# Performance work log

Hardware: AMD Instinct MI355X
Metric: run time of the kernel (lower is better)

Reference implementation:

```python
import jax, jax.numpy as jnp
import numpy as np

B, N, C = 2, 2048, 768
H = 12
HD = C // H  # 64


def setup_inputs() -> dict:
    key = jax.random.key(0)
    ks = jax.random.split(key, 6)
    s = 0.02
    x = jax.random.normal(ks[0], (B, N, C), dtype=jnp.float32)
    xpos = jnp.arange(B * N, dtype=jnp.int64).reshape(B, N) % N
    W_qkv = jax.random.normal(ks[1], (3 * C, C), dtype=jnp.float32) * s
    b_qkv = jnp.zeros((3 * C,), dtype=jnp.float32)
    W_proj = jax.random.normal(ks[2], (C, C), dtype=jnp.float32) * s
    b_proj = jnp.zeros((C,), dtype=jnp.float32)
    return {"x": x, "xpos": xpos, "W_qkv": W_qkv, "b_qkv": b_qkv,
            "W_proj": W_proj, "b_proj": b_proj}


def reference(x, xpos, W_qkv, b_qkv, W_proj, b_proj):
    # rope is None in this configuration -> xpos is unused, matching torch module.
    Bx, Nx, Cx = x.shape
    scale = (Cx // H) ** -0.5
    qkv = x @ W_qkv.T + b_qkv                     # [B, N, 3C]
    qkv = qkv.reshape(Bx, Nx, 3, H, HD)
    q = jnp.einsum('bnhd->bhnd', qkv[:, :, 0])    # [B, H, N, HD]
    k = jnp.einsum('bnhd->bhnd', qkv[:, :, 1])
    v = jnp.einsum('bnhd->bhnd', qkv[:, :, 2])
    attn = jnp.einsum('bhnd,bhmd->bhnm', q, k) * scale  # [B, H, N, N]
    attn = jax.nn.softmax(attn, axis=-1)
    out = jnp.einsum('bhnm,bhmd->bhnd', attn, v)  # [B, H, N, HD]
    out = jnp.einsum('bhnd->bnhd', out).reshape(Bx, Nx, Cx)
    return out @ W_proj.T + b_proj
```

## Files before the change

kernel.cpp:

```cpp
#include <hip/hip_runtime.h>
#include <hip/hip_bf16.h>


typedef _Float16 half8 __attribute__((ext_vector_type(8)));
typedef _Float16 half4_t __attribute__((ext_vector_type(4)));
typedef float floatx4 __attribute__((ext_vector_type(4)));

#define LDA 72
#define LDP 72
#define SCALE_LOG2E 0.1803368801111204f

constexpr int XH_OFF    = 0;
constexpr int WQKV_OFF  = XH_OFF + 4096 * 768;
constexpr int WPROJ_OFF = WQKV_OFF + 2304 * 768;
constexpr int QK_OFF    = WPROJ_OFF + 768 * 768;
constexpr int VTH_OFF   = QK_OFF + 4096 * 1536;

__device__ __forceinline__ void gl16(const _Float16* g, _Float16* l) {
  __builtin_amdgcn_global_load_lds(
      (const __attribute__((address_space(1))) unsigned int*)g,
      (__attribute__((address_space(3))) unsigned int*)l, 16, 0, 0);
}

__global__ __launch_bounds__(256) void cvt_all(const float* __restrict__ x,
                                               const float* __restrict__ wqkv,
                                               const float* __restrict__ wproj,
                                               _Float16* __restrict__ ws) {
  constexpr int n1 = 4096 * 768 / 4;
  constexpr int n2 = 2304 * 768 / 4;
  int i = blockIdx.x * 256 + threadIdx.x;
  const float* src; _Float16* dst; int j;
  if (i < n1)           { src = x;     dst = ws + XH_OFF;    j = i; }
  else if (i < n1 + n2) { src = wqkv;  dst = ws + WQKV_OFF;  j = i - n1; }
  else                  { src = wproj; dst = ws + WPROJ_OFF; j = i - n1 - n2; }
  floatx4 f = *(const floatx4*)(src + 4 * j);
  half4_t h;
  h[0] = (_Float16)f[0]; h[1] = (_Float16)f[1];
  h[2] = (_Float16)f[2]; h[3] = (_Float16)f[3];
  *(half4_t*)(dst + 4 * j) = h;
}

__global__ __launch_bounds__(256) void qkv_gemm(const _Float16* __restrict__ xh,
                                                const _Float16* __restrict__ wh,
                                                const float* __restrict__ bias,
                                                _Float16* __restrict__ qkh,
                                                _Float16* __restrict__ vth) {
  __shared__ __align__(16) _Float16 sA[128 * 64];
  __shared__ __align__(16) _Float16 sB[128 * 64];
  const int tid = threadIdx.x;
  const int nblk = blockIdx.x % 18, mblk = blockIdx.x / 18;
  const int lane = tid & 63, w = tid >> 6;
  const int lane15 = lane & 15, quad = lane >> 4;
  const int wm = w >> 1, wn = w & 1;
  const int lrow = lane >> 3, lchunk = lane & 7;

  const int Abase = mblk * 128 * 768;
  const int Bbase = nblk * 128 * 768;
  const int r0 = w * 32;

  floatx4 acc[4][4];
#pragma unroll
  for (int mt = 0; mt < 4; ++mt)
#pragma unroll
    for (int nt = 0; nt < 4; ++nt) acc[mt][nt] = (floatx4){0.f, 0.f, 0.f, 0.f};

  for (int kt = 0; kt < 12; ++kt) {
    if (kt) __syncthreads();
#pragma unroll
    for (int i = 0; i < 4; ++i) {
      int row = r0 + 8 * i + lrow;
      gl16(xh + Abase + row * 768 + kt * 64 + lchunk * 8, sA + (r0 + 8 * i) * 64);
      gl16(wh + Bbase + row * 768 + kt * 64 + lchunk * 8, sB + (r0 + 8 * i) * 64);
    }
    __syncthreads();
#pragma unroll
    for (int ks = 0; ks < 2; ++ks) {
      half8 af[4], bf[4];
#pragma unroll
      for (int mt = 0; mt < 4; ++mt)
        af[mt] = *(const half8*)(sA + (wm * 64 + mt * 16 + lane15) * 64 + ks * 32 + quad * 8);
#pragma unroll
      for (int nt = 0; nt < 4; ++nt)
        bf[nt] = *(const half8*)(sB + (wn * 64 + nt * 16 + lane15) * 64 + ks * 32 + quad * 8);
#pragma unroll
      for (int mt = 0; mt < 4; ++mt)
#pragma unroll
        for (int nt = 0; nt < 4; ++nt)
          acc[mt][nt] = __builtin_amdgcn_mfma_f32_16x16x32_f16(af[mt], bf[nt], acc[mt][nt], 0, 0, 0);
    }
  }

  const int mbase = mblk * 128 + wm * 64;
  const int nbase = nblk * 128 + wn * 64;
#pragma unroll
  for (int nt = 0; nt < 4; ++nt) {
    int cbase = nbase + nt * 16;
    float bv = bias[cbase + lane15];
    if (cbase < 1536) {
      int col = cbase + lane15;
      float sc = (cbase < 768) ? SCALE_LOG2E : 1.0f;
#pragma unroll
      for (int mt = 0; mt < 4; ++mt)
#pragma unroll
        for (int r = 0; r < 4; ++r) {
          int token = mbase + mt * 16 + quad * 4 + r;
          qkh[token * 1536 + col] = (_Float16)((acc[mt][nt][r] + bv) * sc);
        }
    } else {
      int dcol = cbase - 1536 + lane15;
      int h = dcol >> 6, d = dcol & 63;
#pragma unroll
      for (int mt = 0; mt < 4; ++mt) {
        int tok0 = mbase + mt * 16 + quad * 4;
        int b = tok0 >> 11, n0 = tok0 & 2047;
        int bh = b * 12 + h;
        half4_t hv;
#pragma unroll
        for (int r = 0; r < 4; ++r) hv[r] = (_Float16)(acc[mt][nt][r] + bv);
        *(half4_t*)(vth + (bh * 64 + d) * 2048 + n0) = hv;
      }
    }
  }
}

__global__ __launch_bounds__(256) void attn_fused(const _Float16* __restrict__ qkh,
                                                  const _Float16* __restrict__ vth,
                                                  _Float16* __restrict__ aoh) {
  __shared__ __align__(16) _Float16 sK[64 * LDA];
  __shared__ __align__(16) _Float16 sVT[64 * LDA];
  __shared__ __align__(16) _Float16 sP[4 * 16 * LDP];
  const int tid = threadIdx.x;
  const int bx = blockIdx.x;
  const int bh = bx % 24, qt = bx / 24;
  const int b = bh / 12, h = bh % 12;
  const int lane = tid & 63, w = tid >> 6;
  const int lane15 = lane & 15, quad = lane >> 4;
  const int chunk = tid & 7, rbase = tid >> 3;
  _Float16* sPw = sP + w * 16 * LDP;

  const int qkbase = b * 2048 * 1536 + h * 64;
  const int qrow = qt * 64 + w * 16 + lane15;
  half8 qa0 = *(const half8*)(qkh + qkbase + qrow * 1536 + quad * 8);
  half8 qa1 = *(const half8*)(qkh + qkbase + qrow * 1536 + 32 + quad * 8);

  const _Float16* kptr = qkh + qkbase + 768;
  const _Float16* vptr = vth + bh * 64 * 2048;

  floatx4 O[4];
#pragma unroll
  for (int dt = 0; dt < 4; ++dt) O[dt] = (floatx4){0.f, 0.f, 0.f, 0.f};
  float mrow = -3.0e38f, lrow = 0.f;

  for (int kt = 0; kt < 32; ++kt) {
    half8 tk[2], tv[2];
#pragma unroll
    for (int i = 0; i < 2; ++i) {
      int row = rbase + 32 * i;
      tk[i] = *(const half8*)(kptr + (kt * 64 + row) * 1536 + chunk * 8);
      tv[i] = *(const half8*)(vptr + row * 2048 + kt * 64 + chunk * 8);
    }
    if (kt) __syncthreads();
#pragma unroll
    for (int i = 0; i < 2; ++i) {
      int row = rbase + 32 * i;
      *(half8*)(sK + row * LDA + chunk * 8) = tk[i];
      *(half8*)(sVT + row * LDA + chunk * 8) = tv[i];
    }
    __syncthreads();

    floatx4 s[4];
#pragma unroll
    for (int nt = 0; nt < 4; ++nt) {
      half8 kf0 = *(const half8*)(sK + (nt * 16 + lane15) * LDA + quad * 8);
      half8 kf1 = *(const half8*)(sK + (nt * 16 + lane15) * LDA + 32 + quad * 8);
      floatx4 a = (floatx4){0.f, 0.f, 0.f, 0.f};
      a = __builtin_amdgcn_mfma_f32_16x16x32_f16(kf0, qa0, a, 0, 0, 0);
      a = __builtin_amdgcn_mfma_f32_16x16x32_f16(kf1, qa1, a, 0, 0, 0);
      s[nt] = a;
    }

    float tmax = s[0][0];
#pragma unroll
    for (int nt = 0; nt < 4; ++nt)
#pragma unroll
      for (int r = 0; r < 4; ++r) tmax = fmaxf(tmax, s[nt][r]);
    tmax = fmaxf(tmax, __shfl_xor(tmax, 16, 64));
    tmax = fmaxf(tmax, __shfl_xor(tmax, 32, 64));

    if (__any(tmax > mrow)) {
      float mnew = fmaxf(mrow, tmax);
      float alpha = exp2f(mrow - mnew);
      lrow *= alpha;
      mrow = mnew;
      float ar[4];
#pragma unroll
      for (int r = 0; r < 4; ++r) ar[r] = __shfl(alpha, 4 * quad + r, 64);
#pragma unroll
      for (int dt = 0; dt < 4; ++dt)
#pragma unroll
        for (int r = 0; r < 4; ++r) O[dt][r] *= ar[r];
    }

    float rsum = 0.f;
#pragma unroll
    for (int nt = 0; nt < 4; ++nt)
#pragma unroll
      for (int r = 0; r < 4; ++r) {
        float p = exp2f(s[nt][r] - mrow);
        s[nt][r] = p;
        rsum += p;
      }
    rsum += __shfl_xor(rsum, 16, 64);
    rsum += __shfl_xor(rsum, 32, 64);
    lrow += rsum;

#pragma unroll
    for (int nt = 0; nt < 4; ++nt) {
      half4_t hp;
#pragma unroll
      for (int r = 0; r < 4; ++r) hp[r] = (_Float16)s[nt][r];
      *(half4_t*)(sPw + lane15 * LDP + nt * 16 + quad * 4) = hp;
    }
    asm volatile("s_waitcnt lgkmcnt(0)" ::: "memory");

#pragma unroll
    for (int kk = 0; kk < 2; ++kk) {
      half8 pa = *(const half8*)(sPw + lane15 * LDP + kk * 32 + quad * 8);
#pragma unroll
      for (int dt = 0; dt < 4; ++dt) {
        half8 vb = *(const half8*)(sVT + (dt * 16 + lane15) * LDA + kk * 32 + quad * 8);
        O[dt] = __builtin_amdgcn_mfma_f32_16x16x32_f16(pa, vb, O[dt], 0, 0, 0);
      }
    }
  }

  float inv = 1.0f / lrow;
  float ir[4];
#pragma unroll
  for (int r = 0; r < 4; ++r) ir[r] = __shfl(inv, 4 * quad + r, 64);
#pragma unroll
  for (int dt = 0; dt < 4; ++dt)
#pragma unroll
    for (int r = 0; r < 4; ++r) {
      int tok = qt * 64 + w * 16 + quad * 4 + r;
      aoh[(b * 2048 + tok) * 768 + h * 64 + dt * 16 + lane15] = (_Float16)(O[dt][r] * ir[r]);
    }
}

__global__ __launch_bounds__(256) void proj_gemm(const _Float16* __restrict__ ah,
                                                 const _Float16* __restrict__ wh,
                                                 const float* __restrict__ bias,
                                                 float* __restrict__ out) {
  __shared__ __align__(16) _Float16 sA[128 * 64];
  __shared__ __align__(16) _Float16 sB[128 * 64];
  const int tid = threadIdx.x;
  const int nblk = blockIdx.x % 6, mblk = blockIdx.x / 6;
  const int lane = tid & 63, w = tid >> 6;
  const int lane15 = lane & 15, quad = lane >> 4;
  const int wm = w >> 1, wn = w & 1;
  const int lrow = lane >> 3, lchunk = lane & 7;

  const int Abase = mblk * 128 * 768;
  const int Bbase = nblk * 128 * 768;
  const int r0 = w * 32;

  floatx4 acc[4][4];
#pragma unroll
  for (int mt = 0; mt < 4; ++mt)
#pragma unroll
    for (int nt = 0; nt < 4; ++nt) acc[mt][nt] = (floatx4){0.f, 0.f, 0.f, 0.f};

  for (int kt = 0; kt < 12; ++kt) {
    if (kt) __syncthreads();
#pragma unroll
    for (int i = 0; i < 4; ++i) {
      int row = r0 + 8 * i + lrow;
      gl16(ah + Abase + row * 768 + kt * 64 + lchunk * 8, sA + (r0 + 8 * i) * 64);
      gl16(wh + Bbase + row * 768 + kt * 64 + lchunk * 8, sB + (r0 + 8 * i) * 64);
    }
    __syncthreads();
#pragma unroll
    for (int ks = 0; ks < 2; ++ks) {
      half8 af[4], bf[4];
#pragma unroll
      for (int mt = 0; mt < 4; ++mt)
        af[mt] = *(const half8*)(sA + (wm * 64 + mt * 16 + lane15) * 64 + ks * 32 + quad * 8);
#pragma unroll
      for (int nt = 0; nt < 4; ++nt)
        bf[nt] = *(const half8*)(sB + (wn * 64 + nt * 16 + lane15) * 64 + ks * 32 + quad * 8);
#pragma unroll
      for (int mt = 0; mt < 4; ++mt)
#pragma unroll
        for (int nt = 0; nt < 4; ++nt)
          acc[mt][nt] = __builtin_amdgcn_mfma_f32_16x16x32_f16(af[mt], bf[nt], acc[mt][nt], 0, 0, 0);
    }
  }

  const int mbase = mblk * 128 + wm * 64;
  const int nbase = nblk * 128 + wn * 64;
#pragma unroll
  for (int nt = 0; nt < 4; ++nt) {
    int col = nbase + nt * 16 + lane15;
    float bv = bias[col];
#pragma unroll
    for (int mt = 0; mt < 4; ++mt)
#pragma unroll
      for (int r = 0; r < 4; ++r) {
        int token = mbase + mt * 16 + quad * 4 + r;
        out[token * 768 + col] = acc[mt][nt][r] + bv;
      }
  }
}

extern "C" void kernel_launch(void* const* d_in, const int* in_sizes, int n_in,
                              void* d_out, int out_size, void* d_ws, size_t ws_size,
                              hipStream_t stream) {
  const float* x     = (const float*)d_in[0];
  const float* wqkv  = (const float*)d_in[2];
  const float* bqkv  = (const float*)d_in[3];
  const float* wproj = (const float*)d_in[4];
  const float* bproj = (const float*)d_in[5];
  float* out = (float*)d_out;

  _Float16* ws = (_Float16*)d_ws;
  _Float16* xh     = ws + XH_OFF;
  _Float16* wqkvh  = ws + WQKV_OFF;
  _Float16* wprojh = ws + WPROJ_OFF;
  _Float16* qkh    = ws + QK_OFF;
  _Float16* vth    = ws + VTH_OFF;
  _Float16* aoh    = xh;

  constexpr int total_v4 = (4096 * 768 + 2304 * 768 + 768 * 768) / 4;
  cvt_all<<<total_v4 / 256, 256, 0, stream>>>(x, wqkv, wproj, ws);
  qkv_gemm<<<32 * 18, 256, 0, stream>>>(xh, wqkvh, bqkv, qkh, vth);
  attn_fused<<<24 * 32, 256, 0, stream>>>(qkh, vth, aoh);
  proj_gemm<<<32 * 6, 256, 0, stream>>>(aoh, wprojh, bproj, out);
}
```

Before: 192.3 us.

## Split attention along keys with merge kernel, shrink GEMM M-tiles to 64

The attention kernel now uses 512-thread blocks covering 128 queries and splits the key range into two halves. Each block writes unnormalized partial outputs plus row max and sum to workspace, and a new merge kernel combines the halves with a log-sum-exp rescale. This halves the per-block serial key loop and shares each K/V tile across more queries. Both GEMMs switch to 64x128 tiles with twice as many blocks to improve occupancy and load balance. The cost is an extra kernel launch, extra partial-result traffic to global memory, fp16 rounding of the unnormalized partials, and lower per-block reuse in the GEMMs.

```diff
diff --git a/kernel.cpp b/kernel.cpp
--- a/kernel.cpp
+++ b/kernel.cpp
@@ -15,6 +15,8 @@
 constexpr int WPROJ_OFF = WQKV_OFF + 2304 * 768;
 constexpr int QK_OFF    = WPROJ_OFF + 768 * 768;
 constexpr int VTH_OFF   = QK_OFF + 4096 * 1536;
+constexpr int PO_OFF    = VTH_OFF + 24 * 64 * 2048;
+constexpr int PSTAT_OFF = PO_OFF + 2 * 24 * 2048 * 64;
 
 __device__ __forceinline__ void gl16(const _Float16* g, _Float16* l) {
   __builtin_amdgcn_global_load_lds(
@@ -45,56 +47,53 @@
                                                 const float* __restrict__ bias,
                                                 _Float16* __restrict__ qkh,
                                                 _Float16* __restrict__ vth) {
-  __shared__ __align__(16) _Float16 sA[128 * 64];
+  __shared__ __align__(16) _Float16 sA[64 * 64];
   __shared__ __align__(16) _Float16 sB[128 * 64];
   const int tid = threadIdx.x;
   const int nblk = blockIdx.x % 18, mblk = blockIdx.x / 18;
   const int lane = tid & 63, w = tid >> 6;
   const int lane15 = lane & 15, quad = lane >> 4;
-  const int wm = w >> 1, wn = w & 1;
   const int lrow = lane >> 3, lchunk = lane & 7;
 
-  const int Abase = mblk * 128 * 768;
-  const int Bbase = nblk * 128 * 768;
-  const int r0 = w * 32;
-
-  floatx4 acc[4][4];
+  floatx4 acc[4][2];
 #pragma unroll
   for (int mt = 0; mt < 4; ++mt)
 #pragma unroll
-    for (int nt = 0; nt < 4; ++nt) acc[mt][nt] = (floatx4){0.f, 0.f, 0.f, 0.f};
+    for (int nt = 0; nt < 2; ++nt) acc[mt][nt] = (floatx4){0.f, 0.f, 0.f, 0.f};
 
   for (int kt = 0; kt < 12; ++kt) {
     if (kt) __syncthreads();
 #pragma unroll
-    for (int i = 0; i < 4; ++i) {
-      int row = r0 + 8 * i + lrow;
-      gl16(xh + Abase + row * 768 + kt * 64 + lchunk * 8, sA + (r0 + 8 * i) * 64);
-      gl16(wh + Bbase + row * 768 + kt * 64 + lchunk * 8, sB + (r0 + 8 * i) * 64);
+    for (int i = 0; i < 6; ++i) {
+      int g = w * 48 + 8 * i;
+      if (g < 64)
+        gl16(xh + (mblk * 64 + g + lrow) * 768 + kt * 64 + lchunk * 8, sA + g * 64);
+      else
+        gl16(wh + (nblk * 128 + (g - 64) + lrow) * 768 + kt * 64 + lchunk * 8,
+             sB + (g - 64) * 64);
     }
     __syncthreads();
 #pragma unroll
     for (int ks = 0; ks < 2; ++ks) {
-      half8 af[4], bf[4];
-#pragma unroll
-      for (int mt = 0; mt < 4; ++mt)
-        af[mt] = *(const half8*)(sA + (wm * 64 + mt * 16 + lane15) * 64 + ks * 32 + quad * 8);
-#pragma unroll
-      for (int nt = 0; nt < 4; ++nt)
-        bf[nt] = *(const half8*)(sB + (wn * 64 + nt * 16 + lane15) * 64 + ks * 32 + quad * 8);
-#pragma unroll
-      for (int mt = 0; mt < 4; ++mt)
-#pragma unroll
-        for (int nt = 0; nt < 4; ++nt)
+      half8 af[4], bf[2];
+#pragma unroll
+      for (int mt = 0; mt < 4; ++mt)
+        af[mt] = *(const half8*)(sA + (mt * 16 + lane15) * 64 + ks * 32 + quad * 8);
+#pragma unroll
+      for (int nt = 0; nt < 2; ++nt)
+        bf[nt] = *(const half8*)(sB + (w * 32 + nt * 16 + lane15) * 64 + ks * 32 + quad * 8);
+#pragma unroll
+      for (int mt = 0; mt < 4; ++mt)
+#pragma unroll
+        for (int nt = 0; nt < 2; ++nt)
           acc[mt][nt] = __builtin_amdgcn_mfma_f32_16x16x32_f16(af[mt], bf[nt], acc[mt][nt], 0, 0, 0);
     }
   }
 
-  const int mbase = mblk * 128 + wm * 64;
-  const int nbase = nblk * 128 + wn * 64;
-#pragma unroll
-  for (int nt = 0; nt < 4; ++nt) {
-    int cbase = nbase + nt * 16;
+  const int mbase = mblk * 64;
+#pragma unroll
+  for (int nt = 0; nt < 2; ++nt) {
+    int cbase = nblk * 128 + w * 32 + nt * 16;
     float bv = bias[cbase + lane15];
     if (cbase < 1536) {
       int col = cbase + lane15;
@@ -123,23 +122,28 @@
   }
 }
 
-__global__ __launch_bounds__(256) void attn_fused(const _Float16* __restrict__ qkh,
+__global__ __launch_bounds__(512) void attn_fused(const _Float16* __restrict__ qkh,
                                                   const _Float16* __restrict__ vth,
-                                                  _Float16* __restrict__ aoh) {
+                                                  _Float16* __restrict__ pO,
+                                                  float* __restrict__ pM,
+                                                  float* __restrict__ pL) {
   __shared__ __align__(16) _Float16 sK[64 * LDA];
   __shared__ __align__(16) _Float16 sVT[64 * LDA];
-  __shared__ __align__(16) _Float16 sP[4 * 16 * LDP];
+  __shared__ __align__(16) _Float16 sP[8 * 16 * LDP];
   const int tid = threadIdx.x;
   const int bx = blockIdx.x;
-  const int bh = bx % 24, qt = bx / 24;
+  const int bh = bx % 24;
+  const int rest = bx / 24;
+  const int ks = rest & 1, qt = rest >> 1;
   const int b = bh / 12, h = bh % 12;
   const int lane = tid & 63, w = tid >> 6;
   const int lane15 = lane & 15, quad = lane >> 4;
   const int chunk = tid & 7, rbase = tid >> 3;
+  const int wq = w >> 2, ww = w & 3;
   _Float16* sPw = sP + w * 16 * LDP;
 
   const int qkbase = b * 2048 * 1536 + h * 64;
-  const int qrow = qt * 64 + w * 16 + lane15;
+  const int qrow = qt * 128 + wq * 64 + ww * 16 + lane15;
   half8 qa0 = *(const half8*)(qkh + qkbase + qrow * 1536 + quad * 8);
   half8 qa1 = *(const half8*)(qkh + qkbase + qrow * 1536 + 32 + quad * 8);
 
@@ -151,21 +155,13 @@
   for (int dt = 0; dt < 4; ++dt) O[dt] = (floatx4){0.f, 0.f, 0.f, 0.f};
   float mrow = -3.0e38f, lrow = 0.f;
 
-  for (int kt = 0; kt < 32; ++kt) {
-    half8 tk[2], tv[2];
-#pragma unroll
-    for (int i = 0; i < 2; ++i) {
-      int row = rbase + 32 * i;
-      tk[i] = *(const half8*)(kptr + (kt * 64 + row) * 1536 + chunk * 8);
-      tv[i] = *(const half8*)(vptr + row * 2048 + kt * 64 + chunk * 8);
-    }
-    if (kt) __syncthreads();
-#pragma unroll
-    for (int i = 0; i < 2; ++i) {
-      int row = rbase + 32 * i;
-      *(half8*)(sK + row * LDA + chunk * 8) = tk[i];
-      *(half8*)(sVT + row * LDA + chunk * 8) = tv[i];
-    }
+  const int kt0 = ks * 16;
+  for (int kt = kt0; kt < kt0 + 16; ++kt) {
+    half8 tk = *(const half8*)(kptr + (kt * 64 + rbase) * 1536 + chunk * 8);
+    half8 tv = *(const half8*)(vptr + rbase * 2048 + kt * 64 + chunk * 8);
+    if (kt != kt0) __syncthreads();
+    *(half8*)(sK + rbase * LDA + chunk * 8) = tk;
+    *(half8*)(sVT + rbase * LDA + chunk * 8) = tv;
     __syncthreads();
 
     floatx4 s[4];
@@ -234,73 +230,92 @@
     }
   }
 
-  float inv = 1.0f / lrow;
-  float ir[4];
-#pragma unroll
-  for (int r = 0; r < 4; ++r) ir[r] = __shfl(inv, 4 * quad + r, 64);
+  const int prow = (ks * 24 + bh) * 2048 + qt * 128 + wq * 64 + ww * 16;
 #pragma unroll
   for (int dt = 0; dt < 4; ++dt)
 #pragma unroll
-    for (int r = 0; r < 4; ++r) {
-      int tok = qt * 64 + w * 16 + quad * 4 + r;
-      aoh[(b * 2048 + tok) * 768 + h * 64 + dt * 16 + lane15] = (_Float16)(O[dt][r] * ir[r]);
-    }
+    for (int r = 0; r < 4; ++r)
+      pO[(prow + quad * 4 + r) * 64 + dt * 16 + lane15] = (_Float16)O[dt][r];
+  if (lane < 16) {
+    pM[prow + lane] = mrow;
+    pL[prow + lane] = lrow;
+  }
+}
+
+__global__ __launch_bounds__(256) void attn_merge(const _Float16* __restrict__ pO,
+                                                  const float* __restrict__ pM,
+                                                  const float* __restrict__ pL,
+                                                  _Float16* __restrict__ aoh) {
+  int gid = blockIdx.x * 256 + threadIdx.x;
+  int row = gid >> 3, chunk = gid & 7;
+  int bh = row >> 11, tok = row & 2047;
+  float m1 = pM[row], l1 = pL[row];
+  float m2 = pM[49152 + row], l2 = pL[49152 + row];
+  float M = fmaxf(m1, m2);
+  float f1 = exp2f(m1 - M), f2 = exp2f(m2 - M);
+  float inv = 1.0f / (f1 * l1 + f2 * l2);
+  f1 *= inv; f2 *= inv;
+  half8 o1 = *(const half8*)(pO + row * 64 + chunk * 8);
+  half8 o2 = *(const half8*)(pO + 3145728 + row * 64 + chunk * 8);
+  half8 o;
+#pragma unroll
+  for (int e = 0; e < 8; ++e)
+    o[e] = (_Float16)(f1 * (float)o1[e] + f2 * (float)o2[e]);
+  int b = bh / 12, h = bh % 12;
+  *(half8*)(aoh + (b * 2048 + tok) * 768 + h * 64 + chunk * 8) = o;
 }
 
 __global__ __launch_bounds__(256) void proj_gemm(const _Float16* __restrict__ ah,
                                                  const _Float16* __restrict__ wh,
                                                  const float* __restrict__ bias,
                                                  float* __restrict__ out) {
-  __shared__ __align__(16) _Float16 sA[128 * 64];
+  __shared__ __align__(16) _Float16 sA[64 * 64];
   __shared__ __align__(16) _Float16 sB[128 * 64];
   const int tid = threadIdx.x;
   const int nblk = blockIdx.x % 6, mblk = blockIdx.x / 6;
   const int lane = tid & 63, w = tid >> 6;
   const int lane15 = lane & 15, quad = lane >> 4;
-  const int wm = w >> 1, wn = w & 1;
   const int lrow = lane >> 3, lchunk = lane & 7;
 
-  const int Abase = mblk * 128 * 768;
-  const int Bbase = nblk * 128 * 768;
-  const int r0 = w * 32;
-
-  floatx4 acc[4][4];
+  floatx4 acc[4][2];
 #pragma unroll
   for (int mt = 0; mt < 4; ++mt)
 #pragma unroll
-    for (int nt = 0; nt < 4; ++nt) acc[mt][nt] = (floatx4){0.f, 0.f, 0.f, 0.f};
+    for (int nt = 0; nt < 2; ++nt) acc[mt][nt] = (floatx4){0.f, 0.f, 0.f, 0.f};
 
   for (int kt = 0; kt < 12; ++kt) {
     if (kt) __syncthreads();
 #pragma unroll
-    for (int i = 0; i < 4; ++i) {
-      int row = r0 + 8 * i + lrow;
-      gl16(ah + Abase + row * 768 + kt * 64 + lchunk * 8, sA + (r0 + 8 * i) * 64);
-      gl16(wh + Bbase + row * 768 + kt * 64 + lchunk * 8, sB + (r0 + 8 * i) * 64);
+    for (int i = 0; i < 6; ++i) {
+      int g = w * 48 + 8 * i;
+      if (g < 64)
+        gl16(ah + (mblk * 64 + g + lrow) * 768 + kt * 64 + lchunk * 8, sA + g * 64);
+      else
+        gl16(wh + (nblk * 128 + (g - 64) + lrow) * 768 + kt * 64 + lchunk * 8,
+             sB + (g - 64) * 64);
     }
     __syncthreads();
 #pragma unroll
     for (int ks = 0; ks < 2; ++ks) {
-      half8 af[4], bf[4];
-#pragma unroll
-      for (int mt = 0; mt < 4; ++mt)
-        af[mt] = *(const half8*)(sA + (wm * 64 + mt * 16 + lane15) * 64 + ks * 32 + quad * 8);
-#pragma unroll
-      for (int nt = 0; nt < 4; ++nt)
-        bf[nt] = *(const half8*)(sB + (wn * 64 + nt * 16 + lane15) * 64 + ks * 32 + quad * 8);
-#pragma unroll
-      for (int mt = 0; mt < 4; ++mt)
-#pragma unroll
-        for (int nt = 0; nt < 4; ++nt)
+      half8 af[4], bf[2];
+#pragma unroll
+      for (int mt = 0; mt < 4; ++mt)
+        af[mt] = *(const half8*)(sA + (mt * 16 + lane15) * 64 + ks * 32 + quad * 8);
+#pragma unroll
+      for (int nt = 0; nt < 2; ++nt)
+        bf[nt] = *(const half8*)(sB + (w * 32 + nt * 16 + lane15) * 64 + ks * 32 + quad * 8);
+#pragma unroll
+      for (int mt = 0; mt < 4; ++mt)
+#pragma unroll
+        for (int nt = 0; nt < 2; ++nt)
           acc[mt][nt] = __builtin_amdgcn_mfma_f32_16x16x32_f16(af[mt], bf[nt], acc[mt][nt], 0, 0, 0);
     }
   }
 
-  const int mbase = mblk * 128 + wm * 64;
-  const int nbase = nblk * 128 + wn * 64;
-#pragma unroll
-  for (int nt = 0; nt < 4; ++nt) {
-    int col = nbase + nt * 16 + lane15;
+  const int mbase = mblk * 64;
+#pragma unroll
+  for (int nt = 0; nt < 2; ++nt) {
+    int col = nblk * 128 + w * 32 + nt * 16 + lane15;
     float bv = bias[col];
 #pragma unroll
     for (int mt = 0; mt < 4; ++mt)
@@ -328,11 +343,15 @@
   _Float16* wprojh = ws + WPROJ_OFF;
   _Float16* qkh    = ws + QK_OFF;
   _Float16* vth    = ws + VTH_OFF;
+  _Float16* pO     = ws + PO_OFF;
+  float*    pM     = (float*)(ws + PSTAT_OFF);
+  float*    pL     = pM + 2 * 49152;
   _Float16* aoh    = xh;
 
   constexpr int total_v4 = (4096 * 768 + 2304 * 768 + 768 * 768) / 4;
   cvt_all<<<total_v4 / 256, 256, 0, stream>>>(x, wqkv, wproj, ws);
-  qkv_gemm<<<32 * 18, 256, 0, stream>>>(xh, wqkvh, bqkv, qkh, vth);
-  attn_fused<<<24 * 32, 256, 0, stream>>>(qkh, vth, aoh);
-  proj_gemm<<<32 * 6, 256, 0, stream>>>(aoh, wprojh, bproj, out);
-}
+  qkv_gemm<<<64 * 18, 256, 0, stream>>>(xh, wqkvh, bqkv, qkh, vth);
+  attn_fused<<<24 * 32, 512, 0, stream>>>(qkh, vth, pO, pM, pL);
+  attn_merge<<<1536, 256, 0, stream>>>(pO, pM, pL, aoh);
+  proj_gemm<<<64 * 6, 256, 0, stream>>>(aoh, wprojh, bproj, out);
+}
```

After: 188.4 us. 1.02x faster.
